# Kernel optimization log

Measured on AMD Instinct MI355X. Metric: run time of the kernel, lower is better.

The kernel has to match this reference:

```python
import jax, jax.numpy as jnp
import numpy as np

N = 100000
E = 1200000
C = 64
R = C // 8  # channel-attention reduced dim
G = 256    # number of graphs
EPS = 1e-5


def setup_inputs() -> dict:
    key = jax.random.key(0)
    ks = jax.random.split(key, 12)
    x = jax.random.normal(ks[0], (N, C), dtype=jnp.float32)
    edge_index = jax.random.randint(ks[1], (2, E), 0, N, dtype=jnp.int64)
    batch = jnp.sort(jax.random.randint(ks[2], (N,), 0, G, dtype=jnp.int64))
    s = 1.0 / np.sqrt(C)
    # SAGEConv: lin_l (applied to aggregated neighbors, with bias), lin_r (applied to self, no bias)
    Wl = jax.random.uniform(ks[3], (C, C), jnp.float32, -s, s)
    bl = jax.random.uniform(ks[4], (C,), jnp.float32, -s, s)
    Wr = jax.random.uniform(ks[5], (C, C), jnp.float32, -s, s)
    # GraphNorm params
    gn_w = jnp.ones((C,), jnp.float32)
    gn_b = jnp.zeros((C,), jnp.float32)
    gn_alpha = jnp.ones((C,), jnp.float32)  # mean_scale
    # ChannelAttention params
    sr = 1.0 / np.sqrt(C)
    a1_w = jax.random.uniform(ks[6], (R, C), jnp.float32, -sr, sr)
    a1_b = jax.random.uniform(ks[7], (R,), jnp.float32, -sr, sr)
    s2 = 1.0 / np.sqrt(R)
    a2_w = jax.random.uniform(ks[8], (C, R), jnp.float32, -s2, s2)
    a2_b = jax.random.uniform(ks[9], (C,), jnp.float32, -s2, s2)
    return {"x": x, "edge_index": edge_index, "batch": batch,
            "Wl": Wl, "bl": bl, "Wr": Wr,
            "gn_w": gn_w, "gn_b": gn_b, "gn_alpha": gn_alpha,
            "a1_w": a1_w, "a1_b": a1_b, "a2_w": a2_w, "a2_b": a2_b}


def _sage_conv(x, edge_index, Wl, bl, Wr):
    src, dst = edge_index[0], edge_index[1]
    # mean aggregation of neighbor features at destination nodes
    msg = x[src]  # [E, C]
    agg = jax.ops.segment_sum(msg, dst, num_segments=N)  # [N, C]
    deg = jax.ops.segment_sum(jnp.ones((E,), x.dtype), dst, num_segments=N)
    agg = agg / jnp.maximum(deg, 1.0)[:, None]
    return agg @ Wl.T + bl + x @ Wr.T


def _graph_norm(h, batch, w, b, alpha):
    cnt = jax.ops.segment_sum(jnp.ones((N,), h.dtype), batch, num_segments=G)
    cnt = jnp.maximum(cnt, 1.0)[:, None]  # [G,1]
    mean = jax.ops.segment_sum(h, batch, num_segments=G) / cnt  # [G,C]
    out = h - mean[batch] * alpha
    var = jax.ops.segment_sum(out * out, batch, num_segments=G) / cnt
    return w * out * jax.lax.rsqrt(var[batch] + EPS) + b


def reference(x, edge_index, batch, Wl, bl, Wr, gn_w, gn_b, gn_alpha,
              a1_w, a1_b, a2_w, a2_b):
    tmp = _graph_norm(_sage_conv(x, edge_index, Wl, bl, Wr), batch,
                      gn_w, gn_b, gn_alpha)
    # channel attention gate on the residual branch
    gate = jax.nn.sigmoid(jax.nn.relu(x @ a1_w.T + a1_b) @ a2_w.T + a2_b)
    tmp = tmp + gate * x
    # activation; dropout is identity at eval
    return jax.nn.relu(tmp)
```

## Files before the change

kernel.cpp:

```cpp
#include <hip/hip_runtime.h>
#include <math.h>

#define NN 100000
#define NE 1200000
#define CC 64
#define GG 256
#define RR 8
#define EPSF 1e-5f
#define BINS 782
#define BINP 1024
#define EPB 4688

typedef __attribute__((ext_vector_type(8))) short bf16x8;
typedef __attribute__((ext_vector_type(4))) float f32x4;

__device__ inline unsigned short f2bf(float f) {
  unsigned u = __float_as_uint(f);
  return (unsigned short)((u + 0x7fffu + ((u >> 16) & 1u)) >> 16);
}
__device__ inline float bf2f(unsigned short s) {
  return __uint_as_float(((unsigned)s) << 16);
}

__global__ __launch_bounds__(256) void k_cvt(const float* __restrict__ x,
                                             unsigned short* __restrict__ xb) {
  int i = blockIdx.x * 256 + threadIdx.x;
  if (i >= NN * CC / 8) return;
  const float4* xp = (const float4*)(x + (size_t)i * 8);
  float4 a = xp[0], b = xp[1];
  uint4 o;
  o.x = (unsigned)f2bf(a.x) | ((unsigned)f2bf(a.y) << 16);
  o.y = (unsigned)f2bf(a.z) | ((unsigned)f2bf(a.w) << 16);
  o.z = (unsigned)f2bf(b.x) | ((unsigned)f2bf(b.y) << 16);
  o.w = (unsigned)f2bf(b.z) | ((unsigned)f2bf(b.w) << 16);
  *(uint4*)(xb + (size_t)i * 8) = o;
}

__global__ __launch_bounds__(256) void k_cvtW(const float* __restrict__ Wl,
                                              const float* __restrict__ Wr,
                                              unsigned short* __restrict__ wbl,
                                              unsigned short* __restrict__ wbr) {
  int i = blockIdx.x * 256 + threadIdx.x;
  if (i < CC * CC) {
    wbl[i] = f2bf(Wl[i]);
    wbr[i] = f2bf(Wr[i]);
  }
}

__global__ __launch_bounds__(256) void k_hist(const int* __restrict__ ei,
                                              int* __restrict__ bin_total) {
  __shared__ int hist[BINP];
  for (int t = threadIdx.x; t < BINP; t += 256) hist[t] = 0;
  __syncthreads();
  int start = blockIdx.x * EPB;
  int end = start + EPB < NE ? start + EPB : NE;
  for (int e = start + threadIdx.x; e < end; e += 256)
    atomicAdd(&hist[ei[NE + e] >> 7], 1);
  __syncthreads();
  for (int t = threadIdx.x; t < BINP; t += 256)
    if (hist[t]) atomicAdd(&bin_total[t], hist[t]);
}

__global__ __launch_bounds__(1024) void k_scanbins(const int* __restrict__ bin_total,
                                                   int* __restrict__ bin_base,
                                                   int* __restrict__ cursor,
                                                   int* __restrict__ rowptr) {
  __shared__ int sh[BINP];
  int t = threadIdx.x;
  int v = t < BINS ? bin_total[t] : 0;
  sh[t] = v;
  __syncthreads();
  for (int d = 1; d < BINP; d <<= 1) {
    int val = sh[t];
    int add = (t >= d) ? sh[t - d] : 0;
    __syncthreads();
    sh[t] = val + add;
    __syncthreads();
  }
  int excl = sh[t] - v;
  if (t < BINS) {
    bin_base[t] = excl;
    cursor[t] = excl;
  }
  if (t == 0) {
    bin_base[BINS] = NE;
    rowptr[NN] = NE;
  }
}

__global__ __launch_bounds__(256) void k_phase1(const int* __restrict__ ei,
                                                int* __restrict__ cursor,
                                                unsigned* __restrict__ ebuf) {
  __shared__ int hist[BINP];
  __shared__ int base[BINP];
  for (int t = threadIdx.x; t < BINP; t += 256) hist[t] = 0;
  __syncthreads();
  int start = blockIdx.x * EPB;
  int end = start + EPB < NE ? start + EPB : NE;
  for (int e = start + threadIdx.x; e < end; e += 256)
    atomicAdd(&hist[ei[NE + e] >> 7], 1);
  __syncthreads();
  for (int t = threadIdx.x; t < BINP; t += 256) {
    int c = hist[t];
    base[t] = c ? atomicAdd(&cursor[t], c) : 0;
  }
  __syncthreads();
  for (int t = threadIdx.x; t < BINP; t += 256) hist[t] = 0;
  __syncthreads();
  for (int e = start + threadIdx.x; e < end; e += 256) {
    int src = ei[e], dst = ei[NE + e];
    int b = dst >> 7;
    int off = atomicAdd(&hist[b], 1);
    ebuf[base[b] + off] = ((unsigned)src << 7) | (unsigned)(dst & 127);
  }
}

__global__ __launch_bounds__(256) void k_fill2(const unsigned* __restrict__ ebuf,
                                               const int* __restrict__ bin_base,
                                               int* __restrict__ rowptr,
                                               int* __restrict__ csr) {
  __shared__ int cnt[128];
  __shared__ int sc[128];
  int tid = threadIdx.x;
  int b = blockIdx.x;
  int s = bin_base[b], e = bin_base[b + 1];
  if (tid < 128) cnt[tid] = 0;
  __syncthreads();
  for (int i = s + tid; i < e; i += 256) atomicAdd(&cnt[ebuf[i] & 127], 1);
  __syncthreads();
  if (tid < 128) sc[tid] = cnt[tid];
  __syncthreads();
  for (int d = 1; d < 128; d <<= 1) {
    int v = (tid < 128) ? sc[tid] : 0;
    int a = (tid >= d && tid < 128) ? sc[tid - d] : 0;
    __syncthreads();
    if (tid < 128) sc[tid] = v + a;
    __syncthreads();
  }
  if (tid < 128) {
    sc[tid] -= cnt[tid];
    int node = (b << 7) + tid;
    if (node < NN) rowptr[node] = s + sc[tid];
    cnt[tid] = 0;
  }
  __syncthreads();
  for (int i = s + tid; i < e; i += 256) {
    unsigned v = ebuf[i];
    int dl = v & 127;
    int off = atomicAdd(&cnt[dl], 1);
    csr[s + sc[dl] + off] = (int)(v >> 7) * (CC * 2);
  }
}

__global__ __launch_bounds__(256) void k_gather(const unsigned short* __restrict__ xb,
                                                const int* __restrict__ csr,
                                                const int* __restrict__ rowptr,
                                                unsigned short* __restrict__ aggb) {
  int w = blockIdx.x * 4 + (threadIdx.x >> 6);
  int lane = threadIdx.x & 63;
  if (w >= NN) return;
  int s = rowptr[w], e = rowptr[w + 1];
  const char* xbase = (const char*)xb + lane * 2;
  float acc = 0.0f;
  for (int j0 = s; j0 < e; j0 += 8) {
    int off[8];
#pragma unroll
    for (int u = 0; u < 8; ++u) {
      int j = j0 + u;
      off[u] = csr[j < e ? j : e - 1];
    }
    float v[8];
#pragma unroll
    for (int u = 0; u < 8; ++u)
      v[u] = bf2f(*(const unsigned short*)(xbase + off[u]));
#pragma unroll
    for (int u = 0; u < 8; ++u) acc += (j0 + u < e) ? v[u] : 0.0f;
  }
  float inv = 1.0f / fmaxf((float)(e - s), 1.0f);
  aggb[(size_t)w * CC + lane] = f2bf(acc * inv);
}

__global__ __launch_bounds__(256) void k_passA(
    const unsigned short* __restrict__ xb, const unsigned short* __restrict__ aggb,
    const unsigned short* __restrict__ wbl, const unsigned short* __restrict__ wbr,
    const float* __restrict__ bl, float* __restrict__ h) {
  int lane = threadIdx.x & 63;
  int wave = threadIdx.x >> 6;
  int node0 = blockIdx.x * 64 + wave * 16;
  if (node0 >= NN) return;
  int lr = lane & 15;
  int kg = lane >> 4;

  bf16x8 WL[4][2], WR[4][2];
#pragma unroll
  for (int i = 0; i < 4; ++i)
#pragma unroll
    for (int t = 0; t < 2; ++t) {
      size_t off = (size_t)(i * 16 + lr) * CC + t * 32 + kg * 8;
      WL[i][t] = *(const bf16x8*)(wbl + off);
      WR[i][t] = *(const bf16x8*)(wbr + off);
    }

  int arow = node0 + lr;
  if (arow >= NN) arow = NN - 1;
  bf16x8 Aa[2], Ax[2];
#pragma unroll
  for (int t = 0; t < 2; ++t) {
    Aa[t] = *(const bf16x8*)(aggb + (size_t)arow * CC + t * 32 + kg * 8);
    Ax[t] = *(const bf16x8*)(xb + (size_t)arow * CC + t * 32 + kg * 8);
  }

  f32x4 acc[4];
#pragma unroll
  for (int i = 0; i < 4; ++i) {
    float b = bl[i * 16 + lr];
    acc[i] = (f32x4){b, b, b, b};
  }
#pragma unroll
  for (int i = 0; i < 4; ++i) {
#pragma unroll
    for (int t = 0; t < 2; ++t) {
      acc[i] = __builtin_amdgcn_mfma_f32_16x16x32_bf16(Aa[t], WL[i][t], acc[i], 0, 0, 0);
      acc[i] = __builtin_amdgcn_mfma_f32_16x16x32_bf16(Ax[t], WR[i][t], acc[i], 0, 0, 0);
    }
  }

#pragma unroll
  for (int r = 0; r < 4; ++r) {
    int node = node0 + kg * 4 + r;
    if (node < NN) {
#pragma unroll
      for (int i = 0; i < 4; ++i)
        h[(size_t)node * CC + i * 16 + lr] = acc[i][r];
    }
  }
}

__global__ __launch_bounds__(256) void k_stats(const float* __restrict__ h,
                                               const int* __restrict__ batch,
                                               float* __restrict__ sumH,
                                               float* __restrict__ sumH2,
                                               float* __restrict__ cntg) {
  int w = blockIdx.x * 4 + (threadIdx.x >> 6);
  int lane = threadIdx.x & 63;
  int i0 = w * 16;
  if (i0 >= NN) return;
  int iend = i0 + 16 < NN ? i0 + 16 : NN;
  int gcur = batch[i0];
  float aH = 0.0f, aH2 = 0.0f;
  int run = 0;
  for (int i = i0; i < iend; ++i) {
    int g = batch[i];
    if (g != gcur) {
      atomicAdd(&sumH[(size_t)gcur * CC + lane], aH);
      atomicAdd(&sumH2[(size_t)gcur * CC + lane], aH2);
      if (lane == 0) atomicAdd(&cntg[gcur], (float)run);
      aH = 0.0f; aH2 = 0.0f; run = 0;
      gcur = g;
    }
    float v = h[(size_t)i * CC + lane];
    aH += v;
    aH2 += v * v;
    run++;
  }
  atomicAdd(&sumH[(size_t)gcur * CC + lane], aH);
  atomicAdd(&sumH2[(size_t)gcur * CC + lane], aH2);
  if (lane == 0) atomicAdd(&cntg[gcur], (float)run);
}

__global__ __launch_bounds__(256) void k_passC(
    const float* __restrict__ h, const float* __restrict__ x,
    const int* __restrict__ batch, const float* __restrict__ sumH,
    const float* __restrict__ sumH2, const float* __restrict__ cntg,
    const float* __restrict__ gw, const float* __restrict__ gb,
    const float* __restrict__ alpha, const float* __restrict__ a1w,
    const float* __restrict__ a1b, const float* __restrict__ a2w,
    const float* __restrict__ a2b, float* __restrict__ out) {
  __shared__ float A1[RR * CC];
  __shared__ float A2[CC * RR];
  __shared__ float A1B[RR];
  __shared__ float PRM[4 * CC];
  for (int idx = threadIdx.x; idx < RR * CC; idx += 256) {
    A1[idx] = a1w[idx];
    A2[idx] = a2w[idx];
  }
  if (threadIdx.x < RR) A1B[threadIdx.x] = a1b[threadIdx.x];
  if (threadIdx.x < CC) {
    PRM[threadIdx.x] = a2b[threadIdx.x];
    PRM[CC + threadIdx.x] = gw[threadIdx.x];
    PRM[2 * CC + threadIdx.x] = gb[threadIdx.x];
    PRM[3 * CC + threadIdx.x] = alpha[threadIdx.x];
  }
  __syncthreads();

  int gid = blockIdx.x * 256 + threadIdx.x;
  int i = gid >> 1;
  if (i >= NN) return;
  int half = gid & 1;
  int base = half * 32;
  int g = batch[i];
  float rn = 1.0f / fmaxf(cntg[g], 1.0f);

  float xv[32];
  const float4* xp = (const float4*)(x + (size_t)i * CC + base);
#pragma unroll
  for (int q = 0; q < 8; ++q) {
    float4 b = xp[q];
    xv[4 * q] = b.x; xv[4 * q + 1] = b.y; xv[4 * q + 2] = b.z; xv[4 * q + 3] = b.w;
  }
  float p[RR];
#pragma unroll
  for (int r = 0; r < RR; ++r) {
    float acc = 0.0f;
    const float* a1p = A1 + r * CC + base;
#pragma unroll
    for (int k = 0; k < 32; ++k) acc = fmaf(xv[k], a1p[k], acc);
    acc += __shfl_xor(acc, 1);
    p[r] = fmaxf(acc + A1B[r], 0.0f);
  }
  const float4* hp = (const float4*)(h + (size_t)i * CC + base);
  const float4* sHp = (const float4*)(sumH + (size_t)g * CC + base);
  const float4* sH2p = (const float4*)(sumH2 + (size_t)g * CC + base);
  float4* op = (float4*)(out + (size_t)i * CC + base);
#pragma unroll 4
  for (int q = 0; q < 8; ++q) {
    float4 h4 = hp[q];
    float4 sH = sHp[q];
    float4 sH2 = sH2p[q];
    float hv[4] = {h4.x, h4.y, h4.z, h4.w};
    float sh[4] = {sH.x, sH.y, sH.z, sH.w};
    float sh2[4] = {sH2.x, sH2.y, sH2.z, sH2.w};
    float res[4];
#pragma unroll
    for (int u = 0; u < 4; ++u) {
      int c = base + q * 4 + u;
      float mu = sh[u] * rn;
      float t = PRM[3 * CC + c] * mu;
      float var = sh2[u] * rn - 2.0f * mu * t + t * t;
      float o = hv[u] - t;
      float y = fmaf(PRM[CC + c] * o, rsqrtf(var + EPSF), PRM[2 * CC + c]);
      float gacc = PRM[c];
#pragma unroll
      for (int r = 0; r < RR; ++r) gacc = fmaf(p[r], A2[c * RR + r], gacc);
      float gate = 1.0f / (1.0f + __expf(-gacc));
      res[u] = fmaxf(y + gate * xv[q * 4 + u], 0.0f);
    }
    op[q] = make_float4(res[0], res[1], res[2], res[3]);
  }
}

extern "C" void kernel_launch(void* const* d_in, const int* in_sizes, int n_in,
                              void* d_out, int out_size, void* d_ws, size_t ws_size,
                              hipStream_t stream) {
  const float* x        = (const float*)d_in[0];
  const int*   ei       = (const int*)d_in[1];
  const int*   batch    = (const int*)d_in[2];
  const float* Wl       = (const float*)d_in[3];
  const float* bl       = (const float*)d_in[4];
  const float* Wr       = (const float*)d_in[5];
  const float* gn_w     = (const float*)d_in[6];
  const float* gn_b     = (const float*)d_in[7];
  const float* gn_alpha = (const float*)d_in[8];
  const float* a1w      = (const float*)d_in[9];
  const float* a1b      = (const float*)d_in[10];
  const float* a2w      = (const float*)d_in[11];
  const float* a2b      = (const float*)d_in[12];
  float* out = (float*)d_out;

  float*    h        = (float*)d_ws;
  unsigned* ebuf     = (unsigned*)(h + (size_t)NN * CC);
  int*      csr      = (int*)(ebuf + NE);
  int*      rowptr   = csr + NE;
  int*      bin_tot  = rowptr + NN + 1;
  float*    sumH     = (float*)(bin_tot + BINP);
  float*    sumH2    = sumH + GG * CC;
  float*    cntg     = sumH2 + GG * CC;
  int*      bin_base = (int*)(cntg + GG);
  int*      cursor   = bin_base + BINS + 1;
  unsigned short* wbl = (unsigned short*)(cursor + BINS);
  unsigned short* wbr = wbl + CC * CC;
  unsigned short* xb   = (unsigned short*)d_out;
  unsigned short* aggb = xb + (size_t)NN * CC;

  size_t zbytes = ((size_t)BINP + 2 * GG * CC + GG) * sizeof(int);
  hipMemsetAsync((void*)bin_tot, 0, zbytes, stream);

  k_cvt     <<<(NN * CC / 8 + 255) / 256, 256, 0, stream>>>(x, xb);
  k_cvtW    <<<(CC * CC + 255) / 256, 256, 0, stream>>>(Wl, Wr, wbl, wbr);
  k_hist    <<<256, 256, 0, stream>>>(ei, bin_tot);
  k_scanbins<<<1, BINP, 0, stream>>>(bin_tot, bin_base, cursor, rowptr);
  k_phase1  <<<256, 256, 0, stream>>>(ei, cursor, ebuf);
  k_fill2   <<<BINS, 256, 0, stream>>>(ebuf, bin_base, rowptr, csr);
  k_gather  <<<(NN + 3) / 4, 256, 0, stream>>>(xb, csr, rowptr, aggb);
  k_passA   <<<(NN + 63) / 64, 256, 0, stream>>>(xb, aggb, wbl, wbr, bl, h);
  k_stats   <<<((NN + 15) / 16 + 3) / 4, 256, 0, stream>>>(h, batch, sumH, sumH2, cntg);
  k_passC   <<<(NN * 2 + 255) / 256, 256, 0, stream>>>(h, x, batch, sumH, sumH2, cntg,
                                                       gn_w, gn_b, gn_alpha,
                                                       a1w, a1b, a2w, a2b, out);
}
```

Baseline: 173.2 us.

## Fuse GraphNorm stats into passA, merge weight conversion, widen gather unroll

Computes per-graph sum and sum-of-squares directly from the MFMA accumulators in passA, using a cross-lane shuffle reduction when a 16-node tile lies in a single graph and per-node atomics otherwise. This removes the separate stats kernel and its full re-read of h. The weight bf16 conversion is folded into the x conversion kernel, which drops one launch. The gather loop now issues 16 neighbor loads per iteration instead of 8, raising memory-level parallelism at the cost of more registers and more wasted loads on low-degree nodes.

Result: slower. 181.9 us (+5.0%).

```diff
diff --git a/kernel.cpp b/kernel.cpp
--- a/kernel.cpp
+++ b/kernel.cpp
@@ -23,8 +23,16 @@
 }
 
 __global__ __launch_bounds__(256) void k_cvt(const float* __restrict__ x,
-                                             unsigned short* __restrict__ xb) {
+                                             unsigned short* __restrict__ xb,
+                                             const float* __restrict__ Wl,
+                                             const float* __restrict__ Wr,
+                                             unsigned short* __restrict__ wbl,
+                                             unsigned short* __restrict__ wbr) {
   int i = blockIdx.x * 256 + threadIdx.x;
+  if (i < CC * CC) {
+    wbl[i] = f2bf(Wl[i]);
+    wbr[i] = f2bf(Wr[i]);
+  }
   if (i >= NN * CC / 8) return;
   const float4* xp = (const float4*)(x + (size_t)i * 8);
   float4 a = xp[0], b = xp[1];
@@ -34,17 +42,6 @@
   o.z = (unsigned)f2bf(b.x) | ((unsigned)f2bf(b.y) << 16);
   o.w = (unsigned)f2bf(b.z) | ((unsigned)f2bf(b.w) << 16);
   *(uint4*)(xb + (size_t)i * 8) = o;
-}
-
-__global__ __launch_bounds__(256) void k_cvtW(const float* __restrict__ Wl,
-                                              const float* __restrict__ Wr,
-                                              unsigned short* __restrict__ wbl,
-                                              unsigned short* __restrict__ wbr) {
-  int i = blockIdx.x * 256 + threadIdx.x;
-  if (i < CC * CC) {
-    wbl[i] = f2bf(Wl[i]);
-    wbr[i] = f2bf(Wr[i]);
-  }
 }
 
 __global__ __launch_bounds__(256) void k_hist(const int* __restrict__ ei,
@@ -162,19 +159,19 @@
   int s = rowptr[w], e = rowptr[w + 1];
   const char* xbase = (const char*)xb + lane * 2;
   float acc = 0.0f;
-  for (int j0 = s; j0 < e; j0 += 8) {
-    int off[8];
-#pragma unroll
-    for (int u = 0; u < 8; ++u) {
+  for (int j0 = s; j0 < e; j0 += 16) {
+    int off[16];
+#pragma unroll
+    for (int u = 0; u < 16; ++u) {
       int j = j0 + u;
       off[u] = csr[j < e ? j : e - 1];
     }
-    float v[8];
-#pragma unroll
-    for (int u = 0; u < 8; ++u)
+    float v[16];
+#pragma unroll
+    for (int u = 0; u < 16; ++u)
       v[u] = bf2f(*(const unsigned short*)(xbase + off[u]));
 #pragma unroll
-    for (int u = 0; u < 8; ++u) acc += (j0 + u < e) ? v[u] : 0.0f;
+    for (int u = 0; u < 16; ++u) acc += (j0 + u < e) ? v[u] : 0.0f;
   }
   float inv = 1.0f / fmaxf((float)(e - s), 1.0f);
   aggb[(size_t)w * CC + lane] = f2bf(acc * inv);
@@ -183,7 +180,9 @@
 __global__ __launch_bounds__(256) void k_passA(
     const unsigned short* __restrict__ xb, const unsigned short* __restrict__ aggb,
     const unsigned short* __restrict__ wbl, const unsigned short* __restrict__ wbr,
-    const float* __restrict__ bl, float* __restrict__ h) {
+    const float* __restrict__ bl, float* __restrict__ h,
+    const int* __restrict__ batch, float* __restrict__ sumH,
+    float* __restrict__ sumH2, float* __restrict__ cntg) {
   int lane = threadIdx.x & 63;
   int wave = threadIdx.x >> 6;
   int node0 = blockIdx.x * 64 + wave * 16;
@@ -234,38 +233,49 @@
         h[(size_t)node * CC + i * 16 + lr] = acc[i][r];
     }
   }
-}
-
-__global__ __launch_bounds__(256) void k_stats(const float* __restrict__ h,
-                                               const int* __restrict__ batch,
-                                               float* __restrict__ sumH,
-                                               float* __restrict__ sumH2,
-                                               float* __restrict__ cntg) {
-  int w = blockIdx.x * 4 + (threadIdx.x >> 6);
-  int lane = threadIdx.x & 63;
-  int i0 = w * 16;
-  if (i0 >= NN) return;
-  int iend = i0 + 16 < NN ? i0 + 16 : NN;
-  int gcur = batch[i0];
-  float aH = 0.0f, aH2 = 0.0f;
-  int run = 0;
-  for (int i = i0; i < iend; ++i) {
-    int g = batch[i];
-    if (g != gcur) {
-      atomicAdd(&sumH[(size_t)gcur * CC + lane], aH);
-      atomicAdd(&sumH2[(size_t)gcur * CC + lane], aH2);
-      if (lane == 0) atomicAdd(&cntg[gcur], (float)run);
-      aH = 0.0f; aH2 = 0.0f; run = 0;
-      gcur = g;
-    }
-    float v = h[(size_t)i * CC + lane];
-    aH += v;
-    aH2 += v * v;
-    run++;
-  }
-  atomicAdd(&sumH[(size_t)gcur * CC + lane], aH);
-  atomicAdd(&sumH2[(size_t)gcur * CC + lane], aH2);
-  if (lane == 0) atomicAdd(&cntg[gcur], (float)run);
+
+  int nvalid = NN - node0;
+  if (nvalid > 16) nvalid = 16;
+  int gfirst = batch[node0];
+  int glast = batch[node0 + nvalid - 1];
+  if (gfirst == glast) {
+#pragma unroll
+    for (int i = 0; i < 4; ++i) {
+      float sh = 0.0f, sh2 = 0.0f;
+#pragma unroll
+      for (int r = 0; r < 4; ++r) {
+        int node = node0 + kg * 4 + r;
+        float v = (node < NN) ? acc[i][r] : 0.0f;
+        sh += v;
+        sh2 += v * v;
+      }
+      sh += __shfl_xor(sh, 16);  sh += __shfl_xor(sh, 32);
+      sh2 += __shfl_xor(sh2, 16); sh2 += __shfl_xor(sh2, 32);
+      if (kg == 0) {
+        atomicAdd(&sumH[(size_t)gfirst * CC + i * 16 + lr], sh);
+        atomicAdd(&sumH2[(size_t)gfirst * CC + i * 16 + lr], sh2);
+      }
+    }
+    if (lane == 0) atomicAdd(&cntg[gfirst], (float)nvalid);
+  } else {
+#pragma unroll
+    for (int r = 0; r < 4; ++r) {
+      int node = node0 + kg * 4 + r;
+      if (node < NN) {
+        int g = batch[node];
+#pragma unroll
+        for (int i = 0; i < 4; ++i) {
+          float v = acc[i][r];
+          atomicAdd(&sumH[(size_t)g * CC + i * 16 + lr], v);
+          atomicAdd(&sumH2[(size_t)g * CC + i * 16 + lr], v * v);
+        }
+      }
+    }
+    if (lane == 0) {
+      for (int n = node0; n < node0 + nvalid; ++n)
+        atomicAdd(&cntg[batch[n]], 1.0f);
+    }
+  }
 }
 
 __global__ __launch_bounds__(256) void k_passC(
@@ -385,15 +395,14 @@
   size_t zbytes = ((size_t)BINP + 2 * GG * CC + GG) * sizeof(int);
   hipMemsetAsync((void*)bin_tot, 0, zbytes, stream);
 
-  k_cvt     <<<(NN * CC / 8 + 255) / 256, 256, 0, stream>>>(x, xb);
-  k_cvtW    <<<(CC * CC + 255) / 256, 256, 0, stream>>>(Wl, Wr, wbl, wbr);
+  k_cvt     <<<(NN * CC / 8 + 255) / 256, 256, 0, stream>>>(x, xb, Wl, Wr, wbl, wbr);
   k_hist    <<<256, 256, 0, stream>>>(ei, bin_tot);
   k_scanbins<<<1, BINP, 0, stream>>>(bin_tot, bin_base, cursor, rowptr);
   k_phase1  <<<256, 256, 0, stream>>>(ei, cursor, ebuf);
   k_fill2   <<<BINS, 256, 0, stream>>>(ebuf, bin_base, rowptr, csr);
   k_gather  <<<(NN + 3) / 4, 256, 0, stream>>>(xb, csr, rowptr, aggb);
-  k_passA   <<<(NN + 63) / 64, 256, 0, stream>>>(xb, aggb, wbl, wbr, bl, h);
-  k_stats   <<<((NN + 15) / 16 + 3) / 4, 256, 0, stream>>>(h, batch, sumH, sumH2, cntg);
+  k_passA   <<<(NN + 63) / 64, 256, 0, stream>>>(xb, aggb, wbl, wbr, bl, h,
+                                                 batch, sumH, sumH2, cntg);
   k_passC   <<<(NN * 2 + 255) / 256, 256, 0, stream>>>(h, x, batch, sumH, sumH2, cntg,
                                                        gn_w, gn_b, gn_alpha,
                                                        a1w, a1b, a2w, a2b, out);
```
